# Performance work log

Measured on AMD Instinct MI355X. Metric: run time of the kernel, lower is better.

Reference implementation:

```python
import jax, jax.numpy as jnp
import numpy as np

B, T, C = 4, 2048, 1024
N_HEAD = 16
HEAD_DIM = C // N_HEAD


def setup_inputs() -> dict:
    key = jax.random.key(0)
    k1, k2, k3 = jax.random.split(key, 3)
    x = jax.random.normal(k1, (B, T, C), dtype=jnp.float32)
    # w_attn corresponds to c_attn.weight.T (shape [C, 3C]); w_proj to c_proj.weight.T ([C, C])
    w_attn = jax.random.normal(k2, (C, 3 * C), dtype=jnp.float32) * (1.0 / np.sqrt(C))
    w_proj = jax.random.normal(k3, (C, C), dtype=jnp.float32) * (1.0 / np.sqrt(C))
    return {"x": x, "w_attn": w_attn, "w_proj": w_proj}


def reference(x, w_attn, w_proj):
    Bv, Tv, Cv = x.shape
    qkv = x @ w_attn                                  # [B, T, 3C]
    q, k, v = jnp.split(qkv, 3, axis=-1)
    # [B, T, C] -> [B, H, T, Dh]
    def heads(t):
        return t.reshape(Bv, Tv, N_HEAD, HEAD_DIM).transpose(0, 2, 1, 3)
    q, k, v = heads(q), heads(k), heads(v)
    scale = 1.0 / np.sqrt(HEAD_DIM)
    att = jnp.einsum('bhqd,bhkd->bhqk', q, k) * scale   # [B, H, T, T]
    causal = jnp.tril(jnp.ones((Tv, Tv), dtype=bool))
    att = jnp.where(causal[None, None, :, :], att, -jnp.inf)
    att = jax.nn.softmax(att, axis=-1)
    y = jnp.einsum('bhqk,bhkd->bhqd', att, v)            # [B, H, T, Dh]
    y = y.transpose(0, 2, 1, 3).reshape(Bv, Tv, Cv)      # [B, T, C]
    y = y @ w_proj
    # present_kv = (k, v); return main output y plus cache, matching torch module
    return y, (k, v)
```

## Files before the change

kernel.cpp:

```cpp
#include <hip/hip_runtime.h>

#define B_  4
#define T_  2048
#define C_  1024
#define NH_ 16
#define DH_ 64

typedef __attribute__((ext_vector_type(8))) short bf16x8;
typedef __attribute__((ext_vector_type(4))) float f32x4;

__device__ __forceinline__ unsigned short f2bf(float f) {
  unsigned u = __builtin_bit_cast(unsigned, f);
  u += 0x7fffu + ((u >> 16) & 1u);
  return (unsigned short)(u >> 16);
}

__device__ __forceinline__ void gld16(const void* g, void* l) {
  __builtin_amdgcn_global_load_lds(
      (const __attribute__((address_space(1))) void*)g,
      (__attribute__((address_space(3))) void*)l, 16, 0, 0);
}

__global__ void k_cvt(const float* __restrict__ x, unsigned short* __restrict__ o, int n) {
  int i = (blockIdx.x * 256 + threadIdx.x) * 4;
  if (i < n) {
    const float4 v = *reinterpret_cast<const float4*>(x + i);
    ushort4 u;
    u.x = f2bf(v.x); u.y = f2bf(v.y); u.z = f2bf(v.z); u.w = f2bf(v.w);
    *reinterpret_cast<ushort4*>(o + i) = u;
  }
}

__global__ void k_transpose(const float* __restrict__ w, unsigned short* __restrict__ wt,
                            int K, int N) {
  __shared__ float tile[32][33];
  int tx = threadIdx.x, ty = threadIdx.y;
  int n0 = blockIdx.x * 32, k0 = blockIdx.y * 32;
  #pragma unroll
  for (int j = 0; j < 32; j += 8)
    tile[ty + j][tx] = w[(size_t)(k0 + ty + j) * N + n0 + tx];
  __syncthreads();
  #pragma unroll
  for (int j = 0; j < 32; j += 8)
    wt[(size_t)(n0 + ty + j) * K + k0 + tx] = f2bf(tile[tx][ty + j]);
}

template <int EPI>
__global__ __launch_bounds__(512, 1)
void k_gemm(const unsigned short* __restrict__ A,
            const unsigned short* __restrict__ Bt,
            int M, int N, int K,
            float* __restrict__ outF,
            unsigned short* __restrict__ qb,
            unsigned short* __restrict__ kb,
            unsigned short* __restrict__ vbT,
            float* __restrict__ kout,
            float* __restrict__ vout) {
  __shared__ __align__(16) unsigned short SMEM[49152];

  const int tid  = threadIdx.x;
  const int wave = tid >> 6;
  const int lane = tid & 63;
  const int l15  = lane & 15;
  const int quad = lane >> 4;
  const int wm   = (wave >> 2) * 64;
  const int wn   = (wave & 3) * 64;

  const int gx  = gridDim.x;
  const int lin = blockIdx.y * gx + blockIdx.x;
  const int cpx = (gx * gridDim.y) >> 3;
  const int sw  = (lin & 7) * cpx + (lin >> 3);
  const int m0  = (sw / gx) * 128;
  const int n0  = (sw % gx) * 256;

  const int cof0 = ((quad ^ (l15 & 7)) * 8);
  const int cof1 = cof0 ^ 32;

  f32x4 acc[4][4];
  #pragma unroll
  for (int i = 0; i < 4; i++)
    #pragma unroll
    for (int j = 0; j < 4; j++)
      acc[i][j] = f32x4{0.f, 0.f, 0.f, 0.f};

  auto stage_A = [&](int kt) {
    unsigned short* dst = SMEM + (kt & 1) * 8192;
    const unsigned short* src = A + (size_t)m0 * K + kt * 64;
    #pragma unroll
    for (int it = 0; it < 2; ++it) {
      int c0  = it * 512 + wave * 64;
      int c   = c0 + lane;
      int row = c >> 3;
      int scc = (c & 7) ^ (row & 7);
      gld16(src + (size_t)row * K + scc * 8, dst + c0 * 8);
    }
  };
  auto stage_B = [&](int kt, int h) {
    unsigned short* dst = SMEM + 16384 + (kt & 1) * 16384 + h * 8192;
    const unsigned short* src = Bt + (size_t)(n0 + h * 128) * K + kt * 64;
    #pragma unroll
    for (int it = 0; it < 2; ++it) {
      int c0  = it * 512 + wave * 64;
      int c   = c0 + lane;
      int row = c >> 3;
      int scc = (c & 7) ^ (row & 7);
      gld16(src + (size_t)row * K + scc * 8, dst + c0 * 8);
    }
  };

  const int NT = K >> 6;

  stage_A(0);
  stage_B(0, 0); stage_B(0, 1);
  stage_A(1);
  asm volatile("s_waitcnt vmcnt(2)" ::: "memory");
  __builtin_amdgcn_s_barrier();

  bf16x8 af[4][2], b0[2][2], b1[2][2];

  for (int t = 0; t < NT; ++t) {
    const unsigned short* Au = SMEM + (t & 1) * 8192;
    const unsigned short* Bu = SMEM + 16384 + (t & 1) * 16384;

    #pragma unroll
    for (int mt = 0; mt < 4; mt++) {
      const unsigned short* r = Au + (wm + mt * 16 + l15) * 64;
      af[mt][0] = *reinterpret_cast<const bf16x8*>(r + cof0);
      af[mt][1] = *reinterpret_cast<const bf16x8*>(r + cof1);
    }
    #pragma unroll
    for (int nt = 0; nt < 2; nt++) {
      const unsigned short* r = Bu + (wn + nt * 16 + l15) * 64;
      b0[nt][0] = *reinterpret_cast<const bf16x8*>(r + cof0);
      b0[nt][1] = *reinterpret_cast<const bf16x8*>(r + cof1);
    }
    if (t + 1 < NT) stage_B(t + 1, 0);
    __builtin_amdgcn_s_barrier();
    asm volatile("s_waitcnt lgkmcnt(0)" ::: "memory");
    __builtin_amdgcn_sched_barrier(0);
    __builtin_amdgcn_s_setprio(1);
    #pragma unroll
    for (int mt = 0; mt < 4; mt++)
      #pragma unroll
      for (int nt = 0; nt < 2; nt++) {
        acc[mt][nt] = __builtin_amdgcn_mfma_f32_16x16x32_bf16(af[mt][0], b0[nt][0], acc[mt][nt], 0, 0, 0);
        acc[mt][nt] = __builtin_amdgcn_mfma_f32_16x16x32_bf16(af[mt][1], b0[nt][1], acc[mt][nt], 0, 0, 0);
      }
    __builtin_amdgcn_s_setprio(0);
    __builtin_amdgcn_s_barrier();

    #pragma unroll
    for (int nt = 0; nt < 2; nt++) {
      const unsigned short* r = Bu + (wn + 32 + nt * 16 + l15) * 64;
      b1[nt][0] = *reinterpret_cast<const bf16x8*>(r + cof0);
      b1[nt][1] = *reinterpret_cast<const bf16x8*>(r + cof1);
    }
    if (t + 1 < NT) stage_B(t + 1, 1);
    if (t + 2 < NT) stage_A(t + 2);
    __builtin_amdgcn_s_barrier();
    asm volatile("s_waitcnt lgkmcnt(0)" ::: "memory");
    __builtin_amdgcn_sched_barrier(0);
    __builtin_amdgcn_s_setprio(1);
    #pragma unroll
    for (int mt = 0; mt < 4; mt++)
      #pragma unroll
      for (int nt = 0; nt < 2; nt++) {
        acc[mt][2 + nt] = __builtin_amdgcn_mfma_f32_16x16x32_bf16(af[mt][0], b1[nt][0], acc[mt][2 + nt], 0, 0, 0);
        acc[mt][2 + nt] = __builtin_amdgcn_mfma_f32_16x16x32_bf16(af[mt][1], b1[nt][1], acc[mt][2 + nt], 0, 0, 0);
      }
    __builtin_amdgcn_s_setprio(0);
    if (t + 2 < NT)      { asm volatile("s_waitcnt vmcnt(2)" ::: "memory"); }
    else if (t + 1 < NT) { asm volatile("s_waitcnt vmcnt(0)" ::: "memory"); }
    __builtin_amdgcn_s_barrier();
  }

  if constexpr (EPI == 1) {
    #pragma unroll
    for (int mt = 0; mt < 4; mt++)
      #pragma unroll
      for (int nt = 0; nt < 4; nt++)
        #pragma unroll
        for (int r = 0; r < 4; r++) {
          int gm = m0 + wm + mt * 16 + quad * 4 + r;
          int gn = n0 + wn + nt * 16 + l15;
          outF[(size_t)gm * N + gn] = acc[mt][nt][r];
        }
  } else {
    const int secb = n0 >> 10;
    if (secb == 2) {
      const int b      = m0 >> 11;
      const int t2base = m0 & 2047;
      const int h2base = (n0 - 2048) >> 6;
      #pragma unroll
      for (int mt = 0; mt < 4; mt++)
        #pragma unroll
        for (int nt = 0; nt < 4; nt++) {
          const int col  = wn + nt * 16 + l15;
          const int cn   = (n0 - 2048) + col;
          const int h2   = cn >> 6, d = cn & 63;
          #pragma unroll
          for (int r = 0; r < 4; r++) {
            float v = acc[mt][nt][r];
            int rowl = wm + mt * 16 + quad * 4 + r;
            int t2   = t2base + rowl;
            vout[(((size_t)(b * NH_ + h2)) * T_ + t2) * DH_ + d] = v;
            SMEM[col * 136 + rowl] = f2bf(v);
          }
        }
      __syncthreads();
      #pragma unroll
      for (int i = 0; i < 8; i++) {
        int chunk = i * 512 + tid;
        int col = chunk >> 4, tq = chunk & 15;
        bf16x8 vv = *reinterpret_cast<const bf16x8*>(&SMEM[col * 136 + tq * 8]);
        int h2 = h2base + (col >> 6), d = col & 63;
        size_t idxT = (((size_t)(b * NH_ + h2)) * DH_ + d) * T_ + t2base + tq * 8;
        *reinterpret_cast<bf16x8*>(vbT + idxT) = vv;
      }
    } else {
      #pragma unroll
      for (int mt = 0; mt < 4; mt++)
        #pragma unroll
        for (int nt = 0; nt < 4; nt++)
          #pragma unroll
          for (int r = 0; r < 4; r++) {
            float v  = acc[mt][nt][r];
            int   gm = m0 + wm + mt * 16 + quad * 4 + r;
            int   gn = n0 + wn + nt * 16 + l15;
            int b = gm >> 11, t2 = gm & 2047;
            int cn = gn & 1023;
            int h2 = cn >> 6, d = cn & 63;
            size_t idxN = (((size_t)(b * NH_ + h2)) * T_ + t2) * DH_ + d;
            unsigned short bv = f2bf(v);
            if (secb == 0) { qb[idxN] = bv; }
            else           { kb[idxN] = bv; kout[idxN] = v; }
          }
    }
  }
}

__global__ __launch_bounds__(256, 3)
void k_attn(const unsigned short* __restrict__ qb,
            const unsigned short* __restrict__ kb,
            const unsigned short* __restrict__ vbT,
            unsigned short* __restrict__ ya) {
  __shared__ __align__(16) unsigned short Ks[64 * 64];
  __shared__ __align__(16) unsigned short Vts[64 * 64];
  const int PLD = 72;
  __shared__ __align__(16) unsigned short Ps[4][16 * PLD];

  const int tid  = threadIdx.x;
  const int wave = tid >> 6;
  const int lane = tid & 63;
  const int l15  = lane & 15;
  const int quad = lane >> 4;

  const int blk  = blockIdx.x;
  const int pair = blk & 15;
  const int bh   = blk >> 4;
  const int q0p[2] = {pair * 64, (31 - pair) * 64};
  const int nkt[2] = {pair + 1, 32 - pair};
  const size_t base  = (size_t)bh * T_ * DH_;
  const size_t baseT = (size_t)bh * DH_ * T_;

  const float CS = 0.180336880f;
  const float PB = 17.3123404907f;

  bf16x8 qf[2][2];
  #pragma unroll
  for (int p = 0; p < 2; p++)
    #pragma unroll
    for (int kf = 0; kf < 2; kf++)
      qf[p][kf] = *reinterpret_cast<const bf16x8*>(
          qb + base + (size_t)(q0p[p] + wave * 16 + l15) * DH_ + kf * 32 + quad * 8);

  bf16x8 onesb;
  #pragma unroll
  for (int j = 0; j < 8; j++) onesb[j] = (short)0x3F80;

  f32x4 of[2][4], ls[2];
  #pragma unroll
  for (int p = 0; p < 2; p++) {
    ls[p] = f32x4{0.f, 0.f, 0.f, 0.f};
    #pragma unroll
    for (int nt = 0; nt < 4; nt++)
      of[p][nt] = f32x4{0.f, 0.f, 0.f, 0.f};
  }

  for (int kt = 0; kt < nkt[1]; kt++) {
    __syncthreads();
    #pragma unroll
    for (int i = 0; i < 2; i++) {
      int c0 = (wave * 2 + i) * 64;
      int c  = c0 + lane;
      gld16(kb + base + (size_t)kt * 4096 + (size_t)c * 8, &Ks[c0 * 8]);
      int row = c >> 3, col = c & 7;
      gld16(vbT + baseT + (size_t)row * T_ + kt * 64 + col * 8, &Vts[c0 * 8]);
    }
    __syncthreads();

    bf16x8 bk[4][2], vbf[4][2];
    #pragma unroll
    for (int nt = 0; nt < 4; nt++)
      #pragma unroll
      for (int kf = 0; kf < 2; kf++) {
        bk[nt][kf]  = *reinterpret_cast<const bf16x8*>(&Ks[(nt * 16 + l15) * 64 + kf * 32 + quad * 8]);
        vbf[nt][kf] = *reinterpret_cast<const bf16x8*>(&Vts[(nt * 16 + l15) * 64 + kf * 32 + quad * 8]);
      }

    #pragma unroll
    for (int p = 0; p < 2; p++) {
      if (kt >= nkt[p]) continue;

      f32x4 s[4];
      #pragma unroll
      for (int nt = 0; nt < 4; nt++) s[nt] = f32x4{0.f, 0.f, 0.f, 0.f};
      #pragma unroll
      for (int nt = 0; nt < 4; nt++)
        #pragma unroll
        for (int kf = 0; kf < 2; kf++)
          s[nt] = __builtin_amdgcn_mfma_f32_16x16x32_bf16(qf[p][kf], bk[nt][kf], s[nt], 0, 0, 0);

      if (kt == nkt[p] - 1) {
        #pragma unroll
        for (int nt = 0; nt < 4; nt++) {
          int gk = kt * 64 + nt * 16 + l15;
          #pragma unroll
          for (int r = 0; r < 4; r++) {
            int gq = q0p[p] + wave * 16 + quad * 4 + r;
            s[nt][r] = (gk <= gq) ? s[nt][r] : -3e38f;
          }
        }
      }

      #pragma unroll
      for (int nt = 0; nt < 4; nt++)
        #pragma unroll
        for (int r = 0; r < 4; r++) {
          float pv = __builtin_amdgcn_exp2f(__builtin_fmaf(s[nt][r], CS, -PB));
          Ps[wave][(quad * 4 + r) * PLD + nt * 16 + l15] = f2bf(pv);
        }

      bf16x8 pa[2];
      #pragma unroll
      for (int kf = 0; kf < 2; kf++)
        pa[kf] = *reinterpret_cast<const bf16x8*>(&Ps[wave][l15 * PLD + kf * 32 + quad * 8]);
      #pragma unroll
      for (int nt = 0; nt < 4; nt++)
        #pragma unroll
        for (int kf = 0; kf < 2; kf++)
          of[p][nt] = __builtin_amdgcn_mfma_f32_16x16x32_bf16(pa[kf], vbf[nt][kf], of[p][nt], 0, 0, 0);
      #pragma unroll
      for (int kf = 0; kf < 2; kf++)
        ls[p] = __builtin_amdgcn_mfma_f32_16x16x32_bf16(pa[kf], onesb, ls[p], 0, 0, 0);
    }
  }

  const int b = bh >> 4, h = bh & 15;
  #pragma unroll
  for (int p = 0; p < 2; p++)
    #pragma unroll
    for (int r = 0; r < 4; r++) {
      int t = q0p[p] + wave * 16 + quad * 4 + r;
      float inv = 1.f / ls[p][r];
      #pragma unroll
      for (int nt = 0; nt < 4; nt++) {
        int col = h * DH_ + nt * 16 + l15;
        ya[((size_t)(b * T_ + t)) * C_ + col] = f2bf(of[p][nt][r] * inv);
      }
    }
}

extern "C" void kernel_launch(void* const* d_in, const int* in_sizes, int n_in,
                              void* d_out, int out_size, void* d_ws, size_t ws_size,
                              hipStream_t stream) {
  const float* x      = (const float*)d_in[0];
  const float* w_attn = (const float*)d_in[1];
  const float* w_proj = (const float*)d_in[2];

  float* y    = (float*)d_out;
  float* kout = y + (size_t)B_ * T_ * C_;
  float* vout = kout + (size_t)B_ * T_ * C_;

  char* ws = (char*)d_ws;
  const size_t xe = (size_t)B_ * T_ * C_;
  unsigned short* xb  = (unsigned short*)ws;  ws += xe * 2;
  unsigned short* wab = (unsigned short*)ws;  ws += (size_t)3 * C_ * C_ * 2;
  unsigned short* wpb = (unsigned short*)ws;  ws += (size_t)C_ * C_ * 2;
  unsigned short* qbb = (unsigned short*)ws;  ws += xe * 2;
  unsigned short* kbb = (unsigned short*)ws;  ws += xe * 2;
  unsigned short* vbb = (unsigned short*)ws;  ws += xe * 2;
  unsigned short* ya  = xb;

  const int M = B_ * T_;

  k_cvt<<<(int)(xe / 4 / 256), 256, 0, stream>>>(x, xb, (int)xe);
  k_transpose<<<dim3(3 * C_ / 32, C_ / 32), dim3(32, 8), 0, stream>>>(w_attn, wab, C_, 3 * C_);
  k_transpose<<<dim3(C_ / 32, C_ / 32), dim3(32, 8), 0, stream>>>(w_proj, wpb, C_, C_);

  k_gemm<0><<<dim3(3 * C_ / 256, M / 128), 512, 0, stream>>>(
      xb, wab, M, 3 * C_, C_, nullptr, qbb, kbb, vbb, kout, vout);

  k_attn<<<dim3(B_ * NH_ * 16), 256, 0, stream>>>(qbb, kbb, vbb, ya);

  k_gemm<1><<<dim3(C_ / 256, M / 128), 512, 0, stream>>>(
      ya, wpb, M, C_, C_, y, nullptr, nullptr, nullptr, nullptr, nullptr);
}
```

Before: 327.2 us.

## Double-buffer K/V tiles in attention with XOR-swizzled LDS and MFMA priority

The attention kernel now keeps two LDS buffers for the K and V^T tiles and prefetches the next tile with direct global-to-LDS loads while the current one is computed, leaving one barrier per iteration instead of two. The K/V LDS layout is XOR-swizzled by row so fragment reads avoid bank conflicts. The MFMA sections are wrapped in s_setprio to favour the matrix work. Doubling the K/V buffers raises LDS use per block, which may limit occupancy.

```diff
diff --git a/kernel.cpp b/kernel.cpp
--- a/kernel.cpp
+++ b/kernel.cpp
@@ -244,8 +244,8 @@
             const unsigned short* __restrict__ kb,
             const unsigned short* __restrict__ vbT,
             unsigned short* __restrict__ ya) {
-  __shared__ __align__(16) unsigned short Ks[64 * 64];
-  __shared__ __align__(16) unsigned short Vts[64 * 64];
+  __shared__ __align__(16) unsigned short Ks[2][64 * 64];
+  __shared__ __align__(16) unsigned short Vts[2][64 * 64];
   const int PLD = 72;
   __shared__ __align__(16) unsigned short Ps[4][16 * PLD];
 
@@ -266,6 +266,9 @@
   const float CS = 0.180336880f;
   const float PB = 17.3123404907f;
 
+  const int sco0 = (quad ^ (l15 & 7)) * 8;
+  const int sco1 = sco0 ^ 32;
+
   bf16x8 qf[2][2];
   #pragma unroll
   for (int p = 0; p < 2; p++)
@@ -287,26 +290,41 @@
       of[p][nt] = f32x4{0.f, 0.f, 0.f, 0.f};
   }
 
-  for (int kt = 0; kt < nkt[1]; kt++) {
-    __syncthreads();
+  auto stage = [&](int kt) {
+    unsigned short* dk = Ks[kt & 1];
+    unsigned short* dv = Vts[kt & 1];
     #pragma unroll
     for (int i = 0; i < 2; i++) {
-      int c0 = (wave * 2 + i) * 64;
-      int c  = c0 + lane;
-      gld16(kb + base + (size_t)kt * 4096 + (size_t)c * 8, &Ks[c0 * 8]);
-      int row = c >> 3, col = c & 7;
-      gld16(vbT + baseT + (size_t)row * T_ + kt * 64 + col * 8, &Vts[c0 * 8]);
-    }
-    __syncthreads();
-
+      int c0  = (wave * 2 + i) * 64;
+      int c   = c0 + lane;
+      int row = c >> 3;
+      int sc  = (c & 7) ^ (row & 7);
+      gld16(kb + base + (size_t)(kt * 64 + row) * 64 + sc * 8, dk + c0 * 8);
+      gld16(vbT + baseT + (size_t)row * T_ + kt * 64 + sc * 8, dv + c0 * 8);
+    }
+  };
+
+  const int NT = nkt[1];
+
+  stage(0);
+  asm volatile("s_waitcnt vmcnt(0)" ::: "memory");
+  __builtin_amdgcn_s_barrier();
+
+  for (int kt = 0; kt < NT; kt++) {
+    if (kt + 1 < NT) stage(kt + 1);
+
+    const unsigned short* Ku = Ks[kt & 1];
+    const unsigned short* Vu = Vts[kt & 1];
     bf16x8 bk[4][2], vbf[4][2];
     #pragma unroll
-    for (int nt = 0; nt < 4; nt++)
-      #pragma unroll
-      for (int kf = 0; kf < 2; kf++) {
-        bk[nt][kf]  = *reinterpret_cast<const bf16x8*>(&Ks[(nt * 16 + l15) * 64 + kf * 32 + quad * 8]);
-        vbf[nt][kf] = *reinterpret_cast<const bf16x8*>(&Vts[(nt * 16 + l15) * 64 + kf * 32 + quad * 8]);
-      }
+    for (int nt = 0; nt < 4; nt++) {
+      const unsigned short* rk = Ku + (nt * 16 + l15) * 64;
+      const unsigned short* rv = Vu + (nt * 16 + l15) * 64;
+      bk[nt][0]  = *reinterpret_cast<const bf16x8*>(rk + sco0);
+      bk[nt][1]  = *reinterpret_cast<const bf16x8*>(rk + sco1);
+      vbf[nt][0] = *reinterpret_cast<const bf16x8*>(rv + sco0);
+      vbf[nt][1] = *reinterpret_cast<const bf16x8*>(rv + sco1);
+    }
 
     #pragma unroll
     for (int p = 0; p < 2; p++) {
@@ -315,11 +333,13 @@
       f32x4 s[4];
       #pragma unroll
       for (int nt = 0; nt < 4; nt++) s[nt] = f32x4{0.f, 0.f, 0.f, 0.f};
+      __builtin_amdgcn_s_setprio(1);
       #pragma unroll
       for (int nt = 0; nt < 4; nt++)
         #pragma unroll
         for (int kf = 0; kf < 2; kf++)
           s[nt] = __builtin_amdgcn_mfma_f32_16x16x32_bf16(qf[p][kf], bk[nt][kf], s[nt], 0, 0, 0);
+      __builtin_amdgcn_s_setprio(0);
 
       if (kt == nkt[p] - 1) {
         #pragma unroll
@@ -345,6 +365,7 @@
       #pragma unroll
       for (int kf = 0; kf < 2; kf++)
         pa[kf] = *reinterpret_cast<const bf16x8*>(&Ps[wave][l15 * PLD + kf * 32 + quad * 8]);
+      __builtin_amdgcn_s_setprio(1);
       #pragma unroll
       for (int nt = 0; nt < 4; nt++)
         #pragma unroll
@@ -353,7 +374,11 @@
       #pragma unroll
       for (int kf = 0; kf < 2; kf++)
         ls[p] = __builtin_amdgcn_mfma_f32_16x16x32_bf16(pa[kf], onesb, ls[p], 0, 0, 0);
-    }
+      __builtin_amdgcn_s_setprio(0);
+    }
+
+    asm volatile("s_waitcnt vmcnt(0)" ::: "memory");
+    __builtin_amdgcn_s_barrier();
   }
 
   const int b = bh >> 4, h = bh & 15;
```

Result: faster. 306.0 us (-6.5%).
